# Optimization experiments

Measured on AMD Instinct MI355X. Metric: run time of the kernel, lower is better.

The kernel has to match this reference:

```python
import jax, jax.numpy as jnp
import numpy as np

LN_EPS = 1e-5

def _layer_norm(x, g, b):
    mu = jnp.mean(x, axis=-1, keepdims=True)
    var = jnp.var(x, axis=-1, keepdims=True)
    return (x - mu) * jax.lax.rsqrt(var + LN_EPS) * g + b

def _mlp(x, W1, b1, g1, beta1, W2, b2):
    h = x @ W1 + b1
    h = _layer_norm(h, g1, beta1)
    h = jax.nn.silu(h)
    return h @ W2 + b2

def setup_inputs() -> dict:
    key = jax.random.key(0)
    ks = jax.random.split(key, 16)
    N, E = 50000, 600000
    node_dim, edge_dim, hidden = 128, 128, 256
    def lin(k, fan_in, fan_out):
        bound = 1.0 / np.sqrt(fan_in)
        kw, kb = jax.random.split(k)
        W = jax.random.uniform(kw, (fan_in, fan_out), jnp.float32, -bound, bound)
        b = jax.random.uniform(kb, (fan_out,), jnp.float32, -bound, bound)
        return W, b
    eW1, eb1 = lin(ks[0], 2 * node_dim + edge_dim, hidden)
    eW2, eb2 = lin(ks[1], hidden, edge_dim)
    nW1, nb1 = lin(ks[2], node_dim + edge_dim, hidden)
    nW2, nb2 = lin(ks[3], hidden, node_dim)
    return {
        "node_features": jax.random.normal(ks[4], (N, node_dim), jnp.float32),
        "edge_features": jax.random.normal(ks[5], (E, edge_dim), jnp.float32),
        "edge_index": jax.random.randint(ks[6], (2, E), 0, N, jnp.int64),
        "eW1": eW1, "eb1": eb1, "eg1": jnp.ones((hidden,), jnp.float32), "ebeta1": jnp.zeros((hidden,), jnp.float32),
        "eW2": eW2, "eb2": eb2,
        "nW1": nW1, "nb1": nb1, "ng1": jnp.ones((hidden,), jnp.float32), "nbeta1": jnp.zeros((hidden,), jnp.float32),
        "nW2": nW2, "nb2": nb2,
    }

def reference(node_features, edge_features, edge_index,
              eW1, eb1, eg1, ebeta1, eW2, eb2,
              nW1, nb1, ng1, nbeta1, nW2, nb2):
    senders = edge_index[0]
    receivers = edge_index[1]
    # gather -> edge MLP (residual)
    edge_input = jnp.concatenate(
        [node_features[senders], node_features[receivers], edge_features], axis=-1)  # [E, 2*nd+ed]
    edge_features = edge_features + _mlp(edge_input, eW1, eb1, eg1, ebeta1, eW2, eb2)
    # scatter-add aggregate over receivers
    n_nodes = node_features.shape[0]
    aggregated = jax.ops.segment_sum(edge_features, receivers, num_segments=n_nodes)
    # node MLP (residual)
    node_input = jnp.concatenate([node_features, aggregated], axis=-1)  # [N, nd+ed]
    node_features = node_features + _mlp(node_input, nW1, nb1, ng1, nbeta1, nW2, nb2)
    return node_features, edge_features
```

## Files before the change

kernel.cpp:

```cpp
#include <hip/hip_runtime.h>

#define N_NODES 50000
#define N_EDGES 600000
#define DIM 128
#define HID 256
#define MR 32

typedef float  f32x4  __attribute__((ext_vector_type(4), aligned(16), may_alias));
typedef float  f32x2  __attribute__((ext_vector_type(2), aligned(8),  may_alias));
typedef __bf16 bf16x8 __attribute__((ext_vector_type(8), aligned(16), may_alias));
typedef int    i32x4  __attribute__((ext_vector_type(4), aligned(16), may_alias));

static __device__ inline f32x4 mfma16x16x32(bf16x8 a, bf16x8 b, f32x4 c) {
    return __builtin_amdgcn_mfma_f32_16x16x32_bf16(a, b, c, 0, 0, 0);
}

static __device__ inline bf16x8 cvt2_bf16(f32x4 a, f32x4 b) {
    bf16x8 o;
    o[0] = (__bf16)a[0]; o[1] = (__bf16)a[1]; o[2] = (__bf16)a[2]; o[3] = (__bf16)a[3];
    o[4] = (__bf16)b[0]; o[5] = (__bf16)b[1]; o[6] = (__bf16)b[2]; o[7] = (__bf16)b[3];
    return o;
}

static __device__ inline void pack_one(const float* __restrict__ W,
                                       __bf16* __restrict__ out,
                                       int idx, int Ncols) {
    int lane = idx & 63;
    int tc = idx >> 6;
    int nC = Ncols >> 4;
    int c = tc % nC;
    int t = tc / nC;
    int col = (c << 4) + (lane & 15);
    int k0 = (t << 5) + ((lane >> 4) << 3);
    bf16x8 v;
#pragma unroll
    for (int j = 0; j < 8; ++j) v[j] = (__bf16)W[(k0 + j) * Ncols + col];
    *((bf16x8*)out + idx) = v;
}

__global__ void prep_kernel(const float* __restrict__ node, __bf16* __restrict__ nbf,
                            const float* __restrict__ eW1, const float* __restrict__ eW2,
                            const float* __restrict__ nW1, const float* __restrict__ nW2,
                            __bf16* __restrict__ peW1, __bf16* __restrict__ peW2,
                            __bf16* __restrict__ pnW1, __bf16* __restrict__ pnW2,
                            const int* __restrict__ eidx, int* __restrict__ counts) {
    int b = blockIdx.x;
    if (b < 3125) {
        int idx = b * 256 + threadIdx.x;
        if (idx >= N_NODES * 16) return;
        int row = idx >> 4, c = idx & 15;
        const float* p = node + (size_t)row * DIM + (c << 3);
        f32x4 a = ((const f32x4*)p)[0], bb = ((const f32x4*)p)[1];
        *(bf16x8*)(nbf + (size_t)row * DIM + (c << 3)) = cvt2_bf16(a, bb);
    } else if (b < 3237) {
        int idx = (b - 3125) * 256 + threadIdx.x;
        if (idx < 12288)       pack_one(eW1, peW1, idx, 256);
        else if (idx < 16384)  pack_one(eW2, peW2, idx - 12288, 128);
        else if (idx < 24576)  pack_one(nW1, pnW1, idx - 16384, 256);
        else                   pack_one(nW2, pnW2, idx - 24576, 128);
    } else {
        int e = (b - 3237) * 256 + threadIdx.x;
        if (e < N_EDGES) {
            int r = eidx[N_EDGES + e];
            r = (r < 0) ? 0 : (r >= N_NODES ? N_NODES - 1 : r);
            atomicAdd(&counts[r], 1);
        }
    }
}

__global__ __launch_bounds__(1024) void scan_kernel(const int* __restrict__ counts,
                                                    int* __restrict__ offsets,
                                                    int* __restrict__ cursor) {
    __shared__ int part[1024];
    const int t = threadIdx.x;
    const int CH = (N_NODES + 1023) / 1024;
    const int base = t * CH;
    int s = 0;
#pragma unroll 1
    for (int i = 0; i < CH; ++i) {
        int idx = base + i;
        if (idx < N_NODES) s += counts[idx];
    }
    part[t] = s;
    __syncthreads();
    for (int d = 1; d < 1024; d <<= 1) {
        int x = (t >= d) ? part[t - d] : 0;
        __syncthreads();
        part[t] += x;
        __syncthreads();
    }
    int run = part[t] - s;
#pragma unroll 1
    for (int i = 0; i < CH; ++i) {
        int idx = base + i;
        if (idx < N_NODES) {
            offsets[idx] = run;
            cursor[idx]  = run;
            run += counts[idx];
        }
    }
    if (t == 1023) offsets[N_NODES] = run;
}

__global__ void scatter_kernel(const int* __restrict__ eidx,
                               int* __restrict__ cursor, int* __restrict__ eids) {
    int e = blockIdx.x * 256 + threadIdx.x;
    if (e < N_EDGES) {
        int r = eidx[N_EDGES + e];
        r = (r < 0) ? 0 : (r >= N_NODES ? N_NODES - 1 : r);
        int pos = atomicAdd(&cursor[r], 1);
        eids[pos] = e;
    }
}

__global__ __launch_bounds__(256) void agg_kernel(
    const float* __restrict__ out_edges,
    const int* __restrict__ offsets, const int* __restrict__ eids,
    float* __restrict__ agg) {
    const int tid = threadIdx.x;
    const int n = blockIdx.x * 4 + (tid >> 6);
    const int lane = tid & 63;
    const int es = lane >> 4;
    const int cg = lane & 15;
    float a[8];
#pragma unroll
    for (int j = 0; j < 8; ++j) a[j] = 0.f;
    int st = offsets[n], en = offsets[n + 1];
#pragma unroll 1
    for (int i = st + es; i < en; i += 4) {
        int e = eids[i];
        const float* p = out_edges + (size_t)e * DIM + (cg << 3);
        f32x4 v0 = ((const f32x4*)p)[0], v1 = ((const f32x4*)p)[1];
        a[0] += v0[0]; a[1] += v0[1]; a[2] += v0[2]; a[3] += v0[3];
        a[4] += v1[0]; a[5] += v1[1]; a[6] += v1[2]; a[7] += v1[3];
    }
#pragma unroll
    for (int j = 0; j < 8; ++j) {
        a[j] += __shfl_xor(a[j], 16);
        a[j] += __shfl_xor(a[j], 32);
    }
    if (es == 0) {
        float* q = agg + (size_t)n * DIM + (cg << 3);
        f32x4 w0 = {a[0], a[1], a[2], a[3]};
        f32x4 w1 = {a[4], a[5], a[6], a[7]};
        ((f32x4*)q)[0] = w0;
        ((f32x4*)q)[1] = w1;
    }
}

template<int ASTRIDE, int T1>
__device__ inline void mlp_core(char* lds,
                                const bf16x8* __restrict__ pW1,
                                const bf16x8* __restrict__ pW2,
                                const float* __restrict__ b1,
                                const float* __restrict__ g1,
                                const float* __restrict__ be1,
                                f32x4 (&acc2)[2][2]) {
    const int tid = threadIdx.x;
    const int w = tid >> 6;
    const int lane = tid & 63;
    const int l16 = lane & 15;
    const int g = lane >> 4;
    float* stats = (float*)(lds + 32 * ASTRIDE);

    f32x4 acc[2][4];
#pragma unroll
    for (int m = 0; m < 2; ++m)
#pragma unroll
        for (int n = 0; n < 4; ++n) acc[m][n] = (f32x4){0.f, 0.f, 0.f, 0.f};
#pragma unroll
    for (int t = 0; t < T1; ++t) {
        bf16x8 af[2];
#pragma unroll
        for (int m = 0; m < 2; ++m)
            af[m] = *(const bf16x8*)(lds + (m * 16 + l16) * ASTRIDE + t * 64 + g * 16);
        const bf16x8* bp = pW1 + ((t * 16 + 4 * w) << 6) + lane;
#pragma unroll
        for (int n = 0; n < 4; ++n) {
            bf16x8 bf = bp[n << 6];
#pragma unroll
            for (int m = 0; m < 2; ++m)
                acc[m][n] = mfma16x16x32(af[m], bf, acc[m][n]);
        }
    }

    float b1v[4];
#pragma unroll
    for (int n = 0; n < 4; ++n) b1v[n] = b1[64 * w + 16 * n + l16];
#pragma unroll
    for (int m = 0; m < 2; ++m) {
#pragma unroll
        for (int n = 0; n < 4; ++n) acc[m][n] += b1v[n];
        f32x4 s = (acc[m][0] + acc[m][1]) + (acc[m][2] + acc[m][3]);
        f32x4 q = acc[m][0] * acc[m][0];
        q = acc[m][1] * acc[m][1] + q;
        q = acc[m][2] * acc[m][2] + q;
        q = acc[m][3] * acc[m][3] + q;
#pragma unroll
        for (int st = 1; st <= 8; st <<= 1) {
#pragma unroll
            for (int r = 0; r < 4; ++r) {
                s[r] += __shfl_xor(s[r], st);
                q[r] += __shfl_xor(q[r], st);
            }
        }
        if (l16 == 0) {
#pragma unroll
            for (int r = 0; r < 4; ++r) {
                int row = m * 16 + g * 4 + r;
                *(f32x2*)(stats + row * 8 + w * 2) = (f32x2){s[r], q[r]};
            }
        }
    }
    __syncthreads();

    f32x4 mu4[2], rs4[2];
#pragma unroll
    for (int m = 0; m < 2; ++m)
#pragma unroll
        for (int r = 0; r < 4; ++r) {
            int row = m * 16 + g * 4 + r;
            f32x4 a = *(const f32x4*)(stats + row * 8);
            f32x4 b = *(const f32x4*)(stats + row * 8 + 4);
            float S = (a[0] + a[2]) + (b[0] + b[2]);
            float Q = (a[1] + a[3]) + (b[1] + b[3]);
            float mm = S * (1.f / 256.f);
            float vv = fmaxf(Q * (1.f / 256.f) - mm * mm, 0.f);
            mu4[m][r] = mm;
            rs4[m][r] = __builtin_amdgcn_rsqf(vv + 1e-5f);
        }
    float g1v[4], bev[4];
#pragma unroll
    for (int n = 0; n < 4; ++n) {
        g1v[n] = g1[64 * w + 16 * n + l16];
        bev[n] = be1[64 * w + 16 * n + l16];
    }
#pragma unroll
    for (int m = 0; m < 2; ++m)
#pragma unroll
        for (int n = 0; n < 4; ++n) {
            f32x4 y = (acc[m][n] - mu4[m]) * rs4[m];
            y = y * g1v[n] + bev[n];
            int col = 64 * w + 16 * n + l16;
#pragma unroll
            for (int r = 0; r < 4; ++r) {
                float e = __builtin_amdgcn_exp2f(y[r] * -1.44269504f);
                float x = y[r] * __builtin_amdgcn_rcpf(1.f + e);
                int row = m * 16 + g * 4 + r;
                *(__bf16*)(lds + row * 528 + col * 2) = (__bf16)x;
            }
        }
    __syncthreads();

#pragma unroll
    for (int m = 0; m < 2; ++m)
#pragma unroll
        for (int n = 0; n < 2; ++n) acc2[m][n] = (f32x4){0.f, 0.f, 0.f, 0.f};
#pragma unroll
    for (int t = 0; t < 8; ++t) {
        bf16x8 af[2];
#pragma unroll
        for (int m = 0; m < 2; ++m)
            af[m] = *(const bf16x8*)(lds + (m * 16 + l16) * 528 + t * 64 + g * 16);
        const bf16x8* bp = pW2 + ((t * 8 + 2 * w) << 6) + lane;
#pragma unroll
        for (int n = 0; n < 2; ++n) {
            bf16x8 bf = bp[n << 6];
#pragma unroll
            for (int m = 0; m < 2; ++m)
                acc2[m][n] = mfma16x16x32(af[m], bf, acc2[m][n]);
        }
    }
}

__global__ __launch_bounds__(256, 5) void edge_kernel(
    const __bf16* __restrict__ nbf, const float* __restrict__ ef,
    const int* __restrict__ eidx,
    const bf16x8* __restrict__ pW1, const bf16x8* __restrict__ pW2,
    const float* __restrict__ b1, const float* __restrict__ g1,
    const float* __restrict__ be1, const float* __restrict__ b2,
    float* __restrict__ out_edges) {
    __shared__ __align__(16) char lds[MR * 784 + MR * 32];
    const int tid = threadIdx.x;
    const int eb = blockIdx.x * MR;

    {
        int row = tid >> 3, l8 = tid & 7;
        int e = eb + row;
        int snd = eidx[e], rcv = eidx[N_EDGES + e];
        snd = (snd < 0) ? 0 : (snd >= N_NODES ? N_NODES - 1 : snd);
        rcv = (rcv < 0) ? 0 : (rcv >= N_NODES ? N_NODES - 1 : rcv);
        const char* ps = (const char*)(nbf + (size_t)snd * DIM) + (l8 << 5);
        const char* pr = (const char*)(nbf + (size_t)rcv * DIM) + (l8 << 5);
        char* dst = lds + row * 784 + (l8 << 5);
        *(i32x4*)dst         = *(const i32x4*)ps;
        *(i32x4*)(dst + 16)  = *(const i32x4*)(ps + 16);
        *(i32x4*)(dst + 256) = *(const i32x4*)pr;
        *(i32x4*)(dst + 272) = *(const i32x4*)(pr + 16);
        const float* pe = ef + (size_t)e * DIM + (l8 << 4);
        f32x4 a0 = ((const f32x4*)pe)[0], a1 = ((const f32x4*)pe)[1];
        f32x4 a2 = ((const f32x4*)pe)[2], a3 = ((const f32x4*)pe)[3];
        *(bf16x8*)(dst + 512) = cvt2_bf16(a0, a1);
        *(bf16x8*)(dst + 528) = cvt2_bf16(a2, a3);
    }
    __syncthreads();

    f32x4 acc2[2][2];
    mlp_core<784, 12>(lds, pW1, pW2, b1, g1, be1, acc2);

    {
        const int w = tid >> 6, lane = tid & 63;
        const int l16 = lane & 15, g = lane >> 4;
        float b2v[2];
#pragma unroll
        for (int n = 0; n < 2; ++n) b2v[n] = b2[32 * w + 16 * n + l16];
#pragma unroll
        for (int m = 0; m < 2; ++m)
#pragma unroll
            for (int n = 0; n < 2; ++n)
#pragma unroll
                for (int r = 0; r < 4; ++r) {
                    int e = eb + m * 16 + g * 4 + r;
                    int col = 32 * w + 16 * n + l16;
                    size_t off = (size_t)e * DIM + col;
                    out_edges[off] = acc2[m][n][r] + b2v[n] + ef[off];
                }
    }
}

__global__ __launch_bounds__(256, 5) void node_kernel(
    const float* __restrict__ node, const __bf16* __restrict__ nbf,
    const float* __restrict__ agg,
    const bf16x8* __restrict__ pW1, const bf16x8* __restrict__ pW2,
    const float* __restrict__ b1, const float* __restrict__ g1,
    const float* __restrict__ be1, const float* __restrict__ b2,
    float* __restrict__ out_nodes) {
    __shared__ __align__(16) char lds[MR * 528 + MR * 32];
    const int tid = threadIdx.x;
    const int nb = blockIdx.x * MR;

    {
        int row = tid >> 3, l8 = tid & 7;
        int n = nb + row;
        int nc = (n > N_NODES - 1) ? N_NODES - 1 : n;
        const char* pn = (const char*)(nbf + (size_t)nc * DIM) + (l8 << 5);
        char* dst = lds + row * 528 + (l8 << 5);
        *(i32x4*)dst        = *(const i32x4*)pn;
        *(i32x4*)(dst + 16) = *(const i32x4*)(pn + 16);
        const float* ap = agg + (size_t)nc * DIM + (l8 << 4);
        f32x4 a0 = ((const f32x4*)ap)[0], a1 = ((const f32x4*)ap)[1];
        f32x4 a2 = ((const f32x4*)ap)[2], a3 = ((const f32x4*)ap)[3];
        int cbase = 16 + (l8 << 1);
        *(bf16x8*)(lds + row * 528 + (cbase << 4)) = cvt2_bf16(a0, a1);
        *(bf16x8*)(lds + row * 528 + ((cbase + 1) << 4)) = cvt2_bf16(a2, a3);
    }
    __syncthreads();

    f32x4 acc2[2][2];
    mlp_core<528, 8>(lds, pW1, pW2, b1, g1, be1, acc2);

    {
        const int w = tid >> 6, lane = tid & 63;
        const int l16 = lane & 15, g = lane >> 4;
        float b2v[2];
#pragma unroll
        for (int n = 0; n < 2; ++n) b2v[n] = b2[32 * w + 16 * n + l16];
#pragma unroll
        for (int m = 0; m < 2; ++m)
#pragma unroll
            for (int n = 0; n < 2; ++n)
#pragma unroll
                for (int r = 0; r < 4; ++r) {
                    int nd = nb + m * 16 + g * 4 + r;
                    if (nd < N_NODES) {
                        int col = 32 * w + 16 * n + l16;
                        size_t off = (size_t)nd * DIM + col;
                        out_nodes[off] = acc2[m][n][r] + b2v[n] + node[off];
                    }
                }
    }
}

extern "C" void kernel_launch(void* const* d_in, const int* in_sizes, int n_in,
                              void* d_out, int out_size, void* d_ws, size_t ws_size,
                              hipStream_t stream) {
    const float* node  = (const float*)d_in[0];
    const float* ef    = (const float*)d_in[1];
    const int*   eidx  = (const int*)d_in[2];
    const float* eW1   = (const float*)d_in[3];
    const float* eb1   = (const float*)d_in[4];
    const float* eg1   = (const float*)d_in[5];
    const float* ebt1  = (const float*)d_in[6];
    const float* eW2   = (const float*)d_in[7];
    const float* eb2   = (const float*)d_in[8];
    const float* nW1   = (const float*)d_in[9];
    const float* nb1   = (const float*)d_in[10];
    const float* ng1   = (const float*)d_in[11];
    const float* nbt1  = (const float*)d_in[12];
    const float* nW2   = (const float*)d_in[13];
    const float* nb2   = (const float*)d_in[14];

    char* ws = (char*)d_ws;
    int* counts  = (int*)ws;
    int* offsets = counts + 50016;
    int* cursor  = offsets + 50016;
    int* eids    = cursor + 50016;
    char* abase = (char*)(eids + 600064);
    float* agg = (float*)(((uintptr_t)abase + 255) & ~(uintptr_t)255);
    __bf16* nbf = (__bf16*)(agg + (size_t)N_NODES * DIM);
    __bf16* peW1 = nbf + (size_t)N_NODES * DIM;
    __bf16* peW2 = peW1 + 384 * 256;
    __bf16* pnW1 = peW2 + 256 * 128;
    __bf16* pnW2 = pnW1 + 256 * 256;

    hipMemsetAsync(counts, 0, 50000 * sizeof(int), stream);
    prep_kernel<<<3125 + 112 + 2344, 256, 0, stream>>>(
        node, nbf, eW1, eW2, nW1, nW2, peW1, peW2, pnW1, pnW2, eidx, counts);
    scan_kernel<<<1, 1024, 0, stream>>>(counts, offsets, cursor);
    scatter_kernel<<<(N_EDGES + 255) / 256, 256, 0, stream>>>(eidx, cursor, eids);

    float* out_nodes = (float*)d_out;
    float* out_edges = out_nodes + (size_t)N_NODES * DIM;

    edge_kernel<<<N_EDGES / MR, 256, 0, stream>>>(
        nbf, ef, eidx, (const bf16x8*)peW1, (const bf16x8*)peW2,
        eb1, eg1, ebt1, eb2, out_edges);
    agg_kernel<<<N_NODES / 4, 256, 0, stream>>>(out_edges, offsets, eids, agg);
    node_kernel<<<(N_NODES + MR - 1) / MR, 256, 0, stream>>>(
        node, nbf, agg, (const bf16x8*)pnW1, (const bf16x8*)pnW2,
        nb1, ng1, nbt1, nb2, out_nodes);
}
```

Before: 622.9 us.

## Process two edge tiles per block and prefetch second tile during first MLP

Each edge-kernel block now handles 64 edges as two 32-row tiles. The edge features and indices for the second tile are loaded into registers before the first tile's MLP runs, and its node gathers are written to shared memory before the first tile's outputs are stored. The aim is to hide global-load latency behind MFMA work and to halve the number of blocks. In exchange it raises register pressure under the existing launch bounds and adds extra block-wide barriers.

```diff
diff --git a/kernel.cpp b/kernel.cpp
--- a/kernel.cpp
+++ b/kernel.cpp
@@ -282,10 +282,12 @@
     float* __restrict__ out_edges) {
     __shared__ __align__(16) char lds[MR * 784 + MR * 32];
     const int tid = threadIdx.x;
-    const int eb = blockIdx.x * MR;
-
-    {
-        int row = tid >> 3, l8 = tid & 7;
+    const int row = tid >> 3, l8 = tid & 7;
+    const int eb = blockIdx.x * 64;
+    const int w = tid >> 6, lane = tid & 63;
+    const int l16 = lane & 15, g = lane >> 4;
+
+    {
         int e = eb + row;
         int snd = eidx[e], rcv = eidx[N_EDGES + e];
         snd = (snd < 0) ? 0 : (snd >= N_NODES ? N_NODES - 1 : snd);
@@ -305,12 +307,30 @@
     }
     __syncthreads();
 
+    const int e1 = eb + 32 + row;
+    const float* pe1 = ef + (size_t)e1 * DIM + (l8 << 4);
+    f32x4 c0 = ((const f32x4*)pe1)[0], c1 = ((const f32x4*)pe1)[1];
+    f32x4 c2 = ((const f32x4*)pe1)[2], c3 = ((const f32x4*)pe1)[3];
+    int snd1 = eidx[e1], rcv1 = eidx[N_EDGES + e1];
+    snd1 = (snd1 < 0) ? 0 : (snd1 >= N_NODES ? N_NODES - 1 : snd1);
+    rcv1 = (rcv1 < 0) ? 0 : (rcv1 >= N_NODES ? N_NODES - 1 : rcv1);
+
     f32x4 acc2[2][2];
     mlp_core<784, 12>(lds, pW1, pW2, b1, g1, be1, acc2);
-
-    {
-        const int w = tid >> 6, lane = tid & 63;
-        const int l16 = lane & 15, g = lane >> 4;
+    __syncthreads();
+
+    {
+        const char* ps = (const char*)(nbf + (size_t)snd1 * DIM) + (l8 << 5);
+        const char* pr = (const char*)(nbf + (size_t)rcv1 * DIM) + (l8 << 5);
+        char* dst = lds + row * 784 + (l8 << 5);
+        *(i32x4*)dst         = *(const i32x4*)ps;
+        *(i32x4*)(dst + 16)  = *(const i32x4*)(ps + 16);
+        *(i32x4*)(dst + 256) = *(const i32x4*)pr;
+        *(i32x4*)(dst + 272) = *(const i32x4*)(pr + 16);
+        *(bf16x8*)(dst + 512) = cvt2_bf16(c0, c1);
+        *(bf16x8*)(dst + 528) = cvt2_bf16(c2, c3);
+    }
+    {
         float b2v[2];
 #pragma unroll
         for (int n = 0; n < 2; ++n) b2v[n] = b2[32 * w + 16 * n + l16];
@@ -321,6 +341,26 @@
 #pragma unroll
                 for (int r = 0; r < 4; ++r) {
                     int e = eb + m * 16 + g * 4 + r;
+                    int col = 32 * w + 16 * n + l16;
+                    size_t off = (size_t)e * DIM + col;
+                    out_edges[off] = acc2[m][n][r] + b2v[n] + ef[off];
+                }
+    }
+    __syncthreads();
+
+    mlp_core<784, 12>(lds, pW1, pW2, b1, g1, be1, acc2);
+
+    {
+        float b2v[2];
+#pragma unroll
+        for (int n = 0; n < 2; ++n) b2v[n] = b2[32 * w + 16 * n + l16];
+#pragma unroll
+        for (int m = 0; m < 2; ++m)
+#pragma unroll
+            for (int n = 0; n < 2; ++n)
+#pragma unroll
+                for (int r = 0; r < 4; ++r) {
+                    int e = eb + 32 + m * 16 + g * 4 + r;
                     int col = 32 * w + 16 * n + l16;
                     size_t off = (size_t)e * DIM + col;
                     out_edges[off] = acc2[m][n][r] + b2v[n] + ef[off];
@@ -422,7 +462,7 @@
     float* out_nodes = (float*)d_out;
     float* out_edges = out_nodes + (size_t)N_NODES * DIM;
 
-    edge_kernel<<<N_EDGES / MR, 256, 0, stream>>>(
+    edge_kernel<<<N_EDGES / 64, 256, 0, stream>>>(
         nbf, ef, eidx, (const bf16x8*)peW1, (const bf16x8*)peW2,
         eb1, eg1, ebt1, eb2, out_edges);
     agg_kernel<<<N_NODES / 4, 256, 0, stream>>>(out_edges, offsets, eids, agg);
```

Measured after the change: 1.188 ms. 90.7% more time.
